# Kernel optimization log

Measured on AMD Instinct MI355X. Metric: run time of the kernel, lower is better.

## Reference

```python
import jax, jax.numpy as jnp
import numpy as np

B = 128        # graphs
NPG = 64       # nodes per graph (num_node)
N = B * NPG    # total nodes = 8192
IN = 16        # in_channels
D = 128        # d_model
OUT = 64       # out_channels
CAT = IN * NPG + NPG * NPG  # 5120
EPS = 1e-5


def _lin_init(k, fi, fo):
    s = 1.0 / np.sqrt(fi)
    kw, kb = jax.random.split(k)
    W = jax.random.uniform(kw, (fi, fo), jnp.float32, -s, s)
    b = jax.random.uniform(kb, (fo,), jnp.float32, -s, s)
    return W, b


def setup_inputs() -> dict:
    key = jax.random.key(0)
    ks = jax.random.split(key, 10)
    x = jax.random.normal(ks[0], (N, IN), jnp.float32)
    # complete graph (all i->j pairs, incl. self loops) per graph, offset per graph
    ii = np.repeat(np.arange(NPG), NPG)
    jj = np.tile(np.arange(NPG), NPG)
    off = (np.arange(B) * NPG)[:, None]
    row = (ii[None, :] + off).reshape(-1)
    col = (jj[None, :] + off).reshape(-1)
    edge_index = jnp.asarray(np.stack([row, col]), jnp.int32)  # [2, E]
    E = edge_index.shape[1]
    edge_weight = jax.random.uniform(ks[1], (E,), jnp.float32)
    batch = jnp.repeat(jnp.arange(B, dtype=jnp.int32), NPG)
    W1, b1 = _lin_init(ks[2], IN, D)
    W2, b2 = _lin_init(ks[3], D, D)
    Wm0, bm0 = _lin_init(ks[4], D + CAT, D)
    Wm1, bm1 = _lin_init(ks[5], D, D)
    Wm2, bm2 = _lin_init(ks[6], D, D)
    Wout, bout = _lin_init(ks[7], D, OUT)
    ones = jnp.ones((D,), jnp.float32)
    zeros = jnp.zeros((D,), jnp.float32)
    return dict(x=x, edge_index=edge_index, edge_weight=edge_weight, batch=batch,
                W1=W1, b1=b1, W2=W2, b2=b2,
                Wm0=Wm0, bm0=bm0, g0=ones, be0=zeros,
                Wm1=Wm1, bm1=bm1, g1=ones, be1=zeros,
                Wm2=Wm2, bm2=bm2, g2=ones, be2=zeros,
                Wout=Wout, bout=bout)


def _gcn_conv(h_in, row, col, ew, W, b):
    # PyG GCNConv: linear first, then D^-1/2 (A) D^-1/2 aggregation (self loops already present)
    h = h_in @ W                                             # [N, F]
    deg = jax.ops.segment_sum(ew, col, num_segments=N)       # in-degree by edge weight
    dinv = jnp.where(deg > 0, jax.lax.rsqrt(deg), 0.0)
    norm = dinv[row] * ew * dinv[col]                        # [E]
    out = jax.ops.segment_sum(norm[:, None] * h[row], col, num_segments=N)
    return out + b


def _bn(h, g, b):
    # BatchNorm1d, training-mode math (biased variance), eps=1e-5
    m = jnp.mean(h, axis=0)
    v = jnp.var(h, axis=0)
    return g * (h - m) * jax.lax.rsqrt(v + EPS) + b


def reference(x, edge_index, edge_weight, batch,
              W1, b1, W2, b2,
              Wm0, bm0, g0, be0,
              Wm1, bm1, g1, be1,
              Wm2, bm2, g2, be2,
              Wout, bout):
    row, col = edge_index[0], edge_index[1]
    h = _gcn_conv(x, row, col, edge_weight, W1, b1)
    h = jax.nn.relu(h)
    h = _gcn_conv(h, row, col, edge_weight, W2, b2)
    # global_mean_pool
    sums = jax.ops.segment_sum(h, batch, num_segments=B)
    cnt = jax.ops.segment_sum(jnp.ones((N,), h.dtype), batch, num_segments=B)
    pooled = sums / cnt[:, None]
    pooled = jax.nn.relu(pooled)
    feat = jnp.concatenate([pooled, x.reshape(B, -1), edge_weight.reshape(B, -1)], axis=1)
    feat = jax.nn.relu(feat)
    h = _bn(jax.nn.relu(feat @ Wm0 + bm0), g0, be0)
    h = _bn(jax.nn.relu(h @ Wm1 + bm1), g1, be1)
    h = _bn(jax.nn.relu(h @ Wm2 + bm2), g2, be2)
    return h @ Wout + bout
```

## Files before the change

### kernel.cpp

```cpp
#include <hip/hip_runtime.h>

#define NG 128
#define NPG 64
#define IN 16
#define DM 128
#define NOUT 64
#define EPG 4096
#define NGEMM 160
#define BN_EPS 1e-5f

__global__ __launch_bounds__(256) void k_front(
    const float* __restrict__ x, const float* __restrict__ ew,
    const float* __restrict__ W1, const float* __restrict__ b1,
    const float* __restrict__ Wm0,
    float* __restrict__ z, float* __restrict__ part, float* __restrict__ stats)
{
    __shared__ float u[12544];
    const int b = blockIdx.x, t = threadIdx.x;

    if (b < 256) {
        float* ew_s   = u;
        float* x_s    = u + 4096;
        float* W1h_s  = u + 5120;
        float* P_s    = u + 6144;
        float* b1h_s  = u + 10240;
        float* dinv_s = u + 10304;
        float* t_s    = u + 10368;
        const int g = b >> 1, half = b & 1, fh0 = half * 64;
        if (b == 0) {
            for (int i = t; i < 768; i += 256) stats[i] = 0.f;
        }
        {
            const float4* ew4 = (const float4*)(ew + g * EPG);
            float4* ews4 = (float4*)ew_s;
            #pragma unroll
            for (int i = 0; i < 4; i++) ews4[t + 256 * i] = ew4[t + 256 * i];
            ((float4*)x_s)[t] = ((const float4*)(x + g * NPG * IN))[t];
        }
        for (int i = t; i < IN * 64; i += 256)
            W1h_s[i] = W1[(i >> 6) * DM + fh0 + (i & 63)];
        if (t < 64) b1h_s[t] = b1[fh0 + t];
        __syncthreads();

        if (t < NPG) {
            float s = 0.f;
            #pragma unroll 8
            for (int i = 0; i < NPG; i++) s += ew_s[i * NPG + t];
            dinv_s[t] = (s > 0.f) ? rsqrtf(s) : 0.f;
        }
        __syncthreads();

        {
            const int j = t & 63, q = t >> 6;
            const float dj = dinv_s[j];
            for (int i = q * 16; i < q * 16 + 16; i++) {
                float vv = ew_s[i * NPG + j] * dj;
                #pragma unroll
                for (int off = 32; off > 0; off >>= 1) vv += __shfl_down(vv, off, 64);
                if (j == 0) t_s[i] = dinv_s[i] * vv * (1.f / 64.f);
            }
        }

        {
            const int f = t & 63, ih = t >> 6;
            for (int i = ih * 16; i < ih * 16 + 16; i++) {
                float acc = 0.f;
                #pragma unroll
                for (int k = 0; k < IN; k++) acc += x_s[i * IN + k] * W1h_s[k * 64 + f];
                P_s[i * 64 + f] = acc;
            }
        }
        __syncthreads();

        for (int i = t; i < EPG; i += 256) ew_s[i] *= dinv_s[i >> 6];
        __syncthreads();

        {
            const int j = t & 63, q = t >> 6, fb = q * 16;
            float acc[16];
            #pragma unroll
            for (int uu = 0; uu < 16; uu++) acc[uu] = 0.f;
            for (int i = 0; i < NPG; i++) {
                const float w = ew_s[i * NPG + j];
                const float4* p4 = (const float4*)(P_s + i * 64 + fb);
                #pragma unroll
                for (int u4 = 0; u4 < 4; u4++) {
                    float4 p = p4[u4];
                    acc[4 * u4 + 0] += w * p.x;
                    acc[4 * u4 + 1] += w * p.y;
                    acc[4 * u4 + 2] += w * p.z;
                    acc[4 * u4 + 3] += w * p.w;
                }
            }
            const float dj = dinv_s[j], tj = t_s[j];
            #pragma unroll
            for (int uu = 0; uu < 16; uu++) {
                float h = fmaxf(dj * acc[uu] + b1h_s[fb + uu], 0.f);
                float zv = tj * h;
                #pragma unroll
                for (int off = 32; off > 0; off >>= 1) zv += __shfl_down(zv, off, 64);
                if (j == 0) z[g * DM + fh0 + fb + uu] = zv;
            }
        }
    } else {
        const int c = b - 256;
        const int kc = c >> 1, fh = c & 1;
        float* a_s = u;
        float* b_s = u + 8448;

        const float* src; int stride, off;
        if (kc < 16) { src = x;  stride = 1024; off = kc * 64; }
        else         { src = ew; stride = 4096; off = (kc - 16) * 64; }
        const int K0 = 128 + kc * 64;

        #pragma unroll 4
        for (int it = 0; it < 32; it++) {
            int idx = it * 256 + t;
            int gg = idx >> 6, k = idx & 63;
            a_s[k * 132 + gg] = fmaxf(src[gg * stride + off + k], 0.f);
        }
        #pragma unroll 4
        for (int it = 0; it < 16; it++) {
            int idx = it * 256 + t;
            int k = idx >> 6, fl = idx & 63;
            b_s[k * 64 + fl] = Wm0[(K0 + k) * 128 + fh * 64 + fl];
        }
        __syncthreads();

        const int gthr = t & 31, fthr = t >> 5;
        const int g0 = gthr * 4, f0 = fthr * 8;
        float acc[4][8];
        #pragma unroll
        for (int i = 0; i < 4; i++)
            #pragma unroll
            for (int jx = 0; jx < 8; jx++) acc[i][jx] = 0.f;

        #pragma unroll 4
        for (int k = 0; k < 64; k++) {
            const float4 a4  = *(const float4*)(a_s + k * 132 + g0);
            const float4 c0v = *(const float4*)(b_s + k * 64 + f0);
            const float4 c1v = *(const float4*)(b_s + k * 64 + f0 + 4);
            const float av[4] = {a4.x, a4.y, a4.z, a4.w};
            const float bv[8] = {c0v.x, c0v.y, c0v.z, c0v.w, c1v.x, c1v.y, c1v.z, c1v.w};
            #pragma unroll
            for (int i = 0; i < 4; i++)
                #pragma unroll
                for (int jx = 0; jx < 8; jx++) acc[i][jx] += av[i] * bv[jx];
        }

        float* pp = part + c * 8192;
        #pragma unroll
        for (int i = 0; i < 4; i++) {
            float4* o = (float4*)(pp + (g0 + i) * 64 + f0);
            o[0] = make_float4(acc[i][0], acc[i][1], acc[i][2], acc[i][3]);
            o[1] = make_float4(acc[i][4], acc[i][5], acc[i][6], acc[i][7]);
        }
    }
}

__global__ __launch_bounds__(256) void k_pooled(
    const float* __restrict__ zbuf, const float* __restrict__ W2,
    const float* __restrict__ b2, const float* __restrict__ Wm0,
    float* __restrict__ pooled_part)
{
    __shared__ float W2_s[16384];
    __shared__ float Wm0_s[16384];
    __shared__ float z_s[256];
    __shared__ float pooled_s[2 * 130];
    const int bb = blockIdx.x, t = threadIdx.x, g0 = bb * 2;

    for (int i = t; i < 4096; i += 256) {
        ((float4*)W2_s)[i]  = ((const float4*)W2)[i];
        ((float4*)Wm0_s)[i] = ((const float4*)Wm0)[i];
    }
    if (t < 64) ((float4*)z_s)[t] = ((const float4*)(zbuf + g0 * DM))[t];
    __syncthreads();

    const int cc = t & 127, r = t >> 7;
    float acc = b2[cc];
    #pragma unroll 8
    for (int k = 0; k < DM; k++) acc += z_s[r * DM + k] * W2_s[k * DM + cc];
    pooled_s[r * 130 + cc] = fmaxf(acc, 0.f);
    __syncthreads();

    float acc2 = 0.f;
    #pragma unroll 8
    for (int k = 0; k < DM; k++) acc2 += pooled_s[r * 130 + k] * Wm0_s[k * DM + cc];
    pooled_part[(g0 + r) * DM + cc] = acc2;
}

__global__ __launch_bounds__(256) void k_reduce_bn0(
    const float* __restrict__ part, const float* __restrict__ pooled_part,
    const float* __restrict__ bm0, float* __restrict__ v0,
    float* __restrict__ stats0)
{
    const int bx = blockIdx.x, t = threadIdx.x;
    const int fgrp = bx & 7, gt = bx >> 3;
    const int fsub = t & 15, gl = (t >> 4) & 3, ch = t >> 6;
    const int f = fgrp * 16 + fsub, g = gt * 4 + gl;
    const int fh = f >> 6, fl = f & 63;

    const float* p = part + (size_t)(2 * (ch * 20) + fh) * 8192 + g * 64 + fl;
    float v = 0.f;
    #pragma unroll 5
    for (int cc = 0; cc < 20; cc++) v += p[(size_t)cc * 2 * 8192];

    __shared__ float r1[256];
    r1[t] = v;
    __syncthreads();
    __shared__ float sv[64], sv2[64];
    if (ch == 0) {
        v = r1[t] + r1[t + 64] + r1[t + 128] + r1[t + 192]
          + bm0[f] + pooled_part[g * DM + f];
        v = fmaxf(v, 0.f);
        v0[g * DM + f] = v;
        sv[t] = v; sv2[t] = v * v;
    }
    __syncthreads();
    if (t < 16) {
        float s1 = sv[t] + sv[t + 16] + sv[t + 32] + sv[t + 48];
        float s2 = sv2[t] + sv2[t + 16] + sv2[t + 32] + sv2[t + 48];
        atomicAdd(&stats0[(fgrp * 16 + t) * 2], s1);
        atomicAdd(&stats0[(fgrp * 16 + t) * 2 + 1], s2);
    }
}

__global__ __launch_bounds__(256) void k_mlp(
    const float* __restrict__ vin, const float* __restrict__ statsin,
    const float* __restrict__ gbn, const float* __restrict__ bbn,
    const float* __restrict__ W, const float* __restrict__ bias,
    float* __restrict__ vout, float* __restrict__ statsout)
{
    __shared__ float h_s[128 * 129];
    __shared__ float wcol[128];
    __shared__ float scale_s[128], shift_s[128];
    __shared__ float pc[128];
    __shared__ float rr[4];
    const int f = blockIdx.x, t = threadIdx.x;
    if (t < 128) {
        float s1 = statsin[t * 2], s2 = statsin[t * 2 + 1];
        float m = s1 * (1.f / 128.f);
        float var = s2 * (1.f / 128.f) - m * m;
        float sc = gbn[t] * rsqrtf(var + BN_EPS);
        scale_s[t] = sc;
        shift_s[t] = bbn[t] - m * sc;
        wcol[t] = W[t * 128 + f];
    }
    __syncthreads();
    #pragma unroll 4
    for (int it = 0; it < 64; it++) {
        int idx = it * 256 + t;
        int g = idx >> 7, k = idx & 127;
        h_s[g * 129 + k] = vin[idx] * scale_s[k] + shift_s[k];
    }
    __syncthreads();
    const int g = t & 127, kh = t >> 7;
    float acc = 0.f;
    #pragma unroll 8
    for (int k = kh * 64; k < kh * 64 + 64; k++) acc += h_s[g * 129 + k] * wcol[k];
    if (kh) pc[g] = acc;
    __syncthreads();
    if (t < 128) {
        float v = fmaxf(acc + pc[t] + bias[f], 0.f);
        vout[t * 128 + f] = v;
        float s1 = v, s2 = v * v;
        #pragma unroll
        for (int off = 32; off > 0; off >>= 1) {
            s1 += __shfl_down(s1, off, 64);
            s2 += __shfl_down(s2, off, 64);
        }
        if ((t & 63) == 0) { rr[(t >> 6) * 2] = s1; rr[(t >> 6) * 2 + 1] = s2; }
    }
    __syncthreads();
    if (t == 0) {
        statsout[f * 2]     = rr[0] + rr[2];
        statsout[f * 2 + 1] = rr[1] + rr[3];
    }
}

__global__ __launch_bounds__(128) void k_out(
    const float* __restrict__ vin, const float* __restrict__ statsin,
    const float* __restrict__ gbn, const float* __restrict__ bbn,
    const float* __restrict__ Wo, const float* __restrict__ bo,
    float* __restrict__ out)
{
    __shared__ float Wo_s[128 * 64];
    __shared__ float vrow[2][128];
    __shared__ float scale_s[128], shift_s[128];
    const int b = blockIdx.x, t = threadIdx.x, g0 = b * 2;
    {
        float s1 = statsin[t * 2], s2 = statsin[t * 2 + 1];
        float m = s1 * (1.f / 128.f);
        float var = s2 * (1.f / 128.f) - m * m;
        float sc = gbn[t] * rsqrtf(var + BN_EPS);
        scale_s[t] = sc;
        shift_s[t] = bbn[t] - m * sc;
    }
    __syncthreads();
    #pragma unroll 8
    for (int it = 0; it < 64; it++) {
        int idx = it * 128 + t;
        Wo_s[idx] = Wo[idx];
    }
    #pragma unroll
    for (int it = 0; it < 2; it++) {
        int idx = it * 128 + t;
        int g2 = idx >> 7, k = idx & 127;
        vrow[g2][k] = vin[(g0 + g2) * 128 + k] * scale_s[k] + shift_s[k];
    }
    __syncthreads();
    const int g2 = t >> 6, o = t & 63;
    float acc = bo[o];
    #pragma unroll 8
    for (int k = 0; k < 128; k++) acc += vrow[g2][k] * Wo_s[k * 64 + o];
    out[(g0 + g2) * NOUT + o] = acc;
}

extern "C" void kernel_launch(void* const* d_in, const int* in_sizes, int n_in,
                              void* d_out, int out_size, void* d_ws, size_t ws_size,
                              hipStream_t stream)
{
    const float* x   = (const float*)d_in[0];
    const float* ew  = (const float*)d_in[2];
    const float* W1  = (const float*)d_in[4];
    const float* b1  = (const float*)d_in[5];
    const float* W2  = (const float*)d_in[6];
    const float* b2  = (const float*)d_in[7];
    const float* Wm0 = (const float*)d_in[8];
    const float* bm0 = (const float*)d_in[9];
    const float* g0  = (const float*)d_in[10];
    const float* be0 = (const float*)d_in[11];
    const float* Wm1 = (const float*)d_in[12];
    const float* bm1 = (const float*)d_in[13];
    const float* g1  = (const float*)d_in[14];
    const float* be1 = (const float*)d_in[15];
    const float* Wm2 = (const float*)d_in[16];
    const float* bm2 = (const float*)d_in[17];
    const float* g2  = (const float*)d_in[18];
    const float* be2 = (const float*)d_in[19];
    const float* Wo  = (const float*)d_in[20];
    const float* bo  = (const float*)d_in[21];

    float* ws     = (float*)d_ws;
    float* zbuf   = ws;
    float* part   = zbuf + 16384;
    float* ppart  = part + NGEMM * 8192;
    float* v0     = ppart + 16384;
    float* v1     = v0 + 16384;
    float* v2     = v1 + 16384;
    float* stats  = v2 + 16384;

    k_front<<<256 + NGEMM, 256, 0, stream>>>(x, ew, W1, b1, Wm0, zbuf, part, stats);
    k_pooled<<<64, 256, 0, stream>>>(zbuf, W2, b2, Wm0, ppart);
    k_reduce_bn0<<<256, 256, 0, stream>>>(part, ppart, bm0, v0, stats);
    k_mlp<<<128, 256, 0, stream>>>(v0, stats,       g0, be0, Wm1, bm1, v1, stats + 256);
    k_mlp<<<128, 256, 0, stream>>>(v1, stats + 256, g1, be1, Wm2, bm2, v2, stats + 512);
    k_out<<<NOUT, 128, 0, stream>>>(v2, stats + 512, g2, be2, Wo, bo, (float*)d_out);
}
```

Before: 148.2 us.

## Fuse pooled GCN projection into BN0 reduction kernel and vectorize MLP loads

Removes the separate k_pooled launch. Each k_reduce_bn0 block now recomputes the pooled W2 projection for its 4 graphs and the Wm0 slice for its 16 features, which eliminates one kernel launch and the ppart round trip through global memory. In exchange, every block loads all of W2 (64KB) into LDS and does redundant pooled work, which raises LDS use and may lower occupancy. The k_mlp and k_out input loads are also switched to float4 vector loads.

```diff
diff --git a/kernel.cpp b/kernel.cpp
--- a/kernel.cpp
+++ b/kernel.cpp
@@ -15,7 +15,7 @@
     const float* __restrict__ Wm0,
     float* __restrict__ z, float* __restrict__ part, float* __restrict__ stats)
 {
-    __shared__ float u[12544];
+    __shared__ __align__(16) float u[12544];
     const int b = blockIdx.x, t = threadIdx.x;
 
     if (b < 256) {
@@ -158,42 +158,20 @@
     }
 }
 
-__global__ __launch_bounds__(256) void k_pooled(
-    const float* __restrict__ zbuf, const float* __restrict__ W2,
-    const float* __restrict__ b2, const float* __restrict__ Wm0,
-    float* __restrict__ pooled_part)
-{
-    __shared__ float W2_s[16384];
-    __shared__ float Wm0_s[16384];
-    __shared__ float z_s[256];
-    __shared__ float pooled_s[2 * 130];
-    const int bb = blockIdx.x, t = threadIdx.x, g0 = bb * 2;
-
-    for (int i = t; i < 4096; i += 256) {
-        ((float4*)W2_s)[i]  = ((const float4*)W2)[i];
-        ((float4*)Wm0_s)[i] = ((const float4*)Wm0)[i];
-    }
-    if (t < 64) ((float4*)z_s)[t] = ((const float4*)(zbuf + g0 * DM))[t];
-    __syncthreads();
-
-    const int cc = t & 127, r = t >> 7;
-    float acc = b2[cc];
-    #pragma unroll 8
-    for (int k = 0; k < DM; k++) acc += z_s[r * DM + k] * W2_s[k * DM + cc];
-    pooled_s[r * 130 + cc] = fmaxf(acc, 0.f);
-    __syncthreads();
-
-    float acc2 = 0.f;
-    #pragma unroll 8
-    for (int k = 0; k < DM; k++) acc2 += pooled_s[r * 130 + k] * Wm0_s[k * DM + cc];
-    pooled_part[(g0 + r) * DM + cc] = acc2;
-}
-
 __global__ __launch_bounds__(256) void k_reduce_bn0(
-    const float* __restrict__ part, const float* __restrict__ pooled_part,
-    const float* __restrict__ bm0, float* __restrict__ v0,
-    float* __restrict__ stats0)
-{
+    const float* __restrict__ part, const float* __restrict__ zbuf,
+    const float* __restrict__ W2, const float* __restrict__ b2,
+    const float* __restrict__ Wm0, const float* __restrict__ bm0,
+    float* __restrict__ v0, float* __restrict__ stats0)
+{
+    __shared__ __align__(16) float W2_s[16384];
+    __shared__ __align__(16) float z_s[512];
+    __shared__ float Wm0s[2048];
+    __shared__ float pooled_s[4 * 130];
+    __shared__ float pps[64];
+    __shared__ float r1[256];
+    __shared__ float sv[64], sv2[64];
+
     const int bx = blockIdx.x, t = threadIdx.x;
     const int fgrp = bx & 7, gt = bx >> 3;
     const int fsub = t & 15, gl = (t >> 4) & 3, ch = t >> 6;
@@ -205,13 +183,46 @@
     #pragma unroll 5
     for (int cc = 0; cc < 20; cc++) v += p[(size_t)cc * 2 * 8192];
 
-    __shared__ float r1[256];
+    {
+        const float4* w24 = (const float4*)W2;
+        float4* w2s4 = (float4*)W2_s;
+        #pragma unroll
+        for (int i = 0; i < 16; i++) w2s4[t + 256 * i] = w24[t + 256 * i];
+        if (t < 128) ((float4*)z_s)[t] = ((const float4*)(zbuf + gt * 512))[t];
+        for (int idx = t; idx < 2048; idx += 256) {
+            int k = idx >> 4, fs = idx & 15;
+            Wm0s[idx] = Wm0[k * DM + fgrp * 16 + fs];
+        }
+    }
     r1[t] = v;
     __syncthreads();
-    __shared__ float sv[64], sv2[64];
+
+    {
+        const int gp = t >> 6, k0 = t & 63;
+        float a0 = 0.f, a1 = 0.f;
+        #pragma unroll 4
+        for (int m = 0; m < DM; m++) {
+            const float zm = z_s[gp * DM + m];
+            a0 += zm * W2_s[m * DM + k0];
+            a1 += zm * W2_s[m * DM + k0 + 64];
+        }
+        pooled_s[gp * 130 + k0]      = fmaxf(a0 + b2[k0], 0.f);
+        pooled_s[gp * 130 + k0 + 64] = fmaxf(a1 + b2[k0 + 64], 0.f);
+    }
+    __syncthreads();
+
+    if (t < 64) {
+        const int gl2 = t >> 4, fs = t & 15;
+        float a = 0.f;
+        #pragma unroll 8
+        for (int k = 0; k < DM; k++) a += pooled_s[gl2 * 130 + k] * Wm0s[k * 16 + fs];
+        pps[t] = a;
+    }
+    __syncthreads();
+
     if (ch == 0) {
         v = r1[t] + r1[t + 64] + r1[t + 128] + r1[t + 192]
-          + bm0[f] + pooled_part[g * DM + f];
+          + bm0[f] + pps[t];
         v = fmaxf(v, 0.f);
         v0[g * DM + f] = v;
         sv[t] = v; sv2[t] = v * v;
@@ -248,10 +259,15 @@
     }
     __syncthreads();
     #pragma unroll 4
-    for (int it = 0; it < 64; it++) {
+    for (int it = 0; it < 16; it++) {
         int idx = it * 256 + t;
-        int g = idx >> 7, k = idx & 127;
-        h_s[g * 129 + k] = vin[idx] * scale_s[k] + shift_s[k];
+        int g = idx >> 5, k4 = (idx & 31) * 4;
+        float4 vv = ((const float4*)vin)[idx];
+        float* hp = h_s + g * 129 + k4;
+        hp[0] = vv.x * scale_s[k4 + 0] + shift_s[k4 + 0];
+        hp[1] = vv.y * scale_s[k4 + 1] + shift_s[k4 + 1];
+        hp[2] = vv.z * scale_s[k4 + 2] + shift_s[k4 + 2];
+        hp[3] = vv.w * scale_s[k4 + 3] + shift_s[k4 + 3];
     }
     __syncthreads();
     const int g = t & 127, kh = t >> 7;
@@ -284,7 +300,7 @@
     const float* __restrict__ Wo, const float* __restrict__ bo,
     float* __restrict__ out)
 {
-    __shared__ float Wo_s[128 * 64];
+    __shared__ __align__(16) float Wo_s[128 * 64];
     __shared__ float vrow[2][128];
     __shared__ float scale_s[128], shift_s[128];
     const int b = blockIdx.x, t = threadIdx.x, g0 = b * 2;
@@ -297,16 +313,19 @@
         shift_s[t] = bbn[t] - m * sc;
     }
     __syncthreads();
-    #pragma unroll 8
-    for (int it = 0; it < 64; it++) {
-        int idx = it * 128 + t;
-        Wo_s[idx] = Wo[idx];
-    }
-    #pragma unroll
-    for (int it = 0; it < 2; it++) {
-        int idx = it * 128 + t;
-        int g2 = idx >> 7, k = idx & 127;
-        vrow[g2][k] = vin[(g0 + g2) * 128 + k] * scale_s[k] + shift_s[k];
+    {
+        const float4* wo4 = (const float4*)Wo;
+        float4* wos4 = (float4*)Wo_s;
+        #pragma unroll
+        for (int it = 0; it < 16; it++) wos4[it * 128 + t] = wo4[it * 128 + t];
+    }
+    if (t < 64) {
+        int g2 = t >> 5, k4 = (t & 31) * 4;
+        float4 vv = ((const float4*)(vin + g0 * 128))[t];
+        vrow[g2][k4 + 0] = vv.x * scale_s[k4 + 0] + shift_s[k4 + 0];
+        vrow[g2][k4 + 1] = vv.y * scale_s[k4 + 1] + shift_s[k4 + 1];
+        vrow[g2][k4 + 2] = vv.z * scale_s[k4 + 2] + shift_s[k4 + 2];
+        vrow[g2][k4 + 3] = vv.w * scale_s[k4 + 3] + shift_s[k4 + 3];
     }
     __syncthreads();
     const int g2 = t >> 6, o = t & 63;
@@ -344,15 +363,13 @@
     float* ws     = (float*)d_ws;
     float* zbuf   = ws;
     float* part   = zbuf + 16384;
-    float* ppart  = part + NGEMM * 8192;
-    float* v0     = ppart + 16384;
+    float* v0     = part + NGEMM * 8192;
     float* v1     = v0 + 16384;
     float* v2     = v1 + 16384;
     float* stats  = v2 + 16384;
 
     k_front<<<256 + NGEMM, 256, 0, stream>>>(x, ew, W1, b1, Wm0, zbuf, part, stats);
-    k_pooled<<<64, 256, 0, stream>>>(zbuf, W2, b2, Wm0, ppart);
-    k_reduce_bn0<<<256, 256, 0, stream>>>(part, ppart, bm0, v0, stats);
+    k_reduce_bn0<<<256, 256, 0, stream>>>(part, zbuf, W2, b2, Wm0, bm0, v0, stats);
     k_mlp<<<128, 256, 0, stream>>>(v0, stats,       g0, be0, Wm1, bm1, v1, stats + 256);
     k_mlp<<<128, 256, 0, stream>>>(v1, stats + 256, g1, be1, Wm2, bm2, v2, stats + 512);
     k_out<<<NOUT, 128, 0, stream>>>(v2, stats + 512, g2, be2, Wo, bo, (float*)d_out);
```

Measured after the change: 140.4 us. 1.06x faster.
